# Performance work log

Hardware: AMD Instinct MI355X
Metric: run time of the kernel (lower is better)

The kernel has to match this reference:

```python
import jax, jax.numpy as jnp
import numpy as np

N_NODES = 65536
N_EDGES = 262144
N_GRAPHS = 2048
NF = 16   # num_node_features
EF = 6    # num_edge_features
H1, H2, H3 = 32, 16, 8  # conv1 out, conv2 out, lin1 out


def _lin_init(key, fan_in, fan_out):
    kw, kb = jax.random.split(key)
    s = 1.0 / np.sqrt(fan_in)
    w = jax.random.uniform(kw, (fan_in, fan_out), minval=-s, maxval=s, dtype=jnp.float32)
    b = jax.random.uniform(kb, (fan_out,), minval=-s, maxval=s, dtype=jnp.float32)
    return w, b


def setup_inputs() -> dict:
    key = jax.random.key(0)
    ks = jax.random.split(key, 16)
    inp = {}
    inp["x_p"] = jax.random.normal(ks[0], (N_NODES, NF), dtype=jnp.float32)
    inp["x_d"] = jax.random.normal(ks[1], (4, NF), dtype=jnp.float32)  # unused by forward
    inp["edge_attr_p"] = jax.random.uniform(ks[2], (N_EDGES, EF), dtype=jnp.float32)
    inp["edge_attr_d"] = jax.random.uniform(ks[3], (4, EF), dtype=jnp.float32)  # unused
    inp["edge_index_p"] = jax.random.randint(ks[4], (2, N_EDGES), 0, N_NODES, dtype=jnp.int32)
    inp["x_p_batch"] = jnp.sort(jax.random.randint(ks[5], (N_NODES,), 0, N_GRAPHS, dtype=jnp.int32))
    # conv1: NNConv(NF, 32); edge nn: Linear(EF,16) -> ReLU -> Linear(16, NF*32)
    inp["nn1_w1"], inp["nn1_b1"] = _lin_init(ks[6], EF, 16)
    inp["nn1_w2"], inp["nn1_b2"] = _lin_init(ks[7], 16, NF * H1)
    inp["root1"] = _lin_init(ks[8], NF, H1)[0]
    inp["bias1"] = jnp.zeros((H1,), dtype=jnp.float32)
    # conv2: NNConv(32, 16); edge nn: Linear(EF,16) -> ReLU -> Linear(16, 32*16)
    inp["nn2_w1"], inp["nn2_b1"] = _lin_init(ks[9], EF, 16)
    inp["nn2_w2"], inp["nn2_b2"] = _lin_init(ks[10], 16, H1 * H2)
    inp["root2"] = _lin_init(ks[11], H1, H2)[0]
    inp["bias2"] = jnp.zeros((H2,), dtype=jnp.float32)
    # attention pooling gate: Linear(NF,NF) -> ReLU -> Linear(NF,1)
    inp["gate_w1"], inp["gate_b1"] = _lin_init(ks[12], NF, NF)
    inp["gate_w2"], inp["gate_b2"] = _lin_init(ks[13], NF, 1)
    # head: Linear(16+16, 8) -> Linear(8, 1)  (attention=True)
    inp["lin1_w"], inp["lin1_b"] = _lin_init(ks[14], H2 + NF, H3)
    inp["lin2_w"], inp["lin2_b"] = _lin_init(ks[15], H3, 1)
    return inp


def _nnconv(x, edge_attr, src, dst, w1, b1, w2, b2, root, bias, in_c, out_c, n_nodes):
    # per-edge dynamic weight matrix Theta(e) : [E, in_c, out_c]
    h = jax.nn.relu(edge_attr @ w1 + b1) @ w2 + b2
    w_dyn = h.reshape(-1, in_c, out_c)
    msg = jnp.einsum('ei,eio->eo', x[src], w_dyn)          # [E, out_c]
    agg = jax.ops.segment_sum(msg, dst, num_segments=n_nodes)  # scatter-add
    return agg + x @ root + bias


def _attention_pool(x, batch, gw1, gb1, gw2, gb2, n_graphs):
    g = (jax.nn.relu(x @ gw1 + gb1) @ gw2 + gb2)[:, 0]     # [N] gate logits
    m = jax.ops.segment_max(g, batch, num_segments=n_graphs)
    e = jnp.exp(g - m[batch])
    s = jax.ops.segment_sum(e, batch, num_segments=n_graphs)
    alpha = e / s[batch]                                    # per-graph softmax
    return jax.ops.segment_sum(alpha[:, None] * x, batch, num_segments=n_graphs)


def _mean_pool(x, batch, n_graphs):
    s = jax.ops.segment_sum(x, batch, num_segments=n_graphs)
    cnt = jax.ops.segment_sum(jnp.ones((x.shape[0],), x.dtype), batch, num_segments=n_graphs)
    return s / jnp.maximum(cnt, 1.0)[:, None]


def reference(x_p, x_d, edge_attr_p, edge_attr_d, edge_index_p, x_p_batch,
              nn1_w1, nn1_b1, nn1_w2, nn1_b2, root1, bias1,
              nn2_w1, nn2_b1, nn2_w2, nn2_b2, root2, bias2,
              gate_w1, gate_b1, gate_w2, gate_b2,
              lin1_w, lin1_b, lin2_w, lin2_b):
    src, dst = edge_index_p[0], edge_index_p[1]
    # attention pooling on raw node features (attention=True)
    x_att = _attention_pool(x_p, x_p_batch, gate_w1, gate_b1, gate_w2, gate_b2, N_GRAPHS)
    # two NNConv layers with ReLU
    h = jax.nn.relu(_nnconv(x_p, edge_attr_p, src, dst, nn1_w1, nn1_b1, nn1_w2, nn1_b2,
                            root1, bias1, NF, H1, N_NODES))
    h = jax.nn.relu(_nnconv(h, edge_attr_p, src, dst, nn2_w1, nn2_b1, nn2_w2, nn2_b2,
                            root2, bias2, H1, H2, N_NODES))
    g = _mean_pool(h, x_p_batch, N_GRAPHS)                  # [B, 16]
    g = jnp.concatenate([g, x_att], axis=1)                 # [B, 32]
    # dropout p=0.5 is identity in eval mode
    g = g @ lin1_w + lin1_b
    out = g @ lin2_w + lin2_b                               # [B, 1]
    return out
```

## Files before the change

### kernel.cpp

```cpp
#include <hip/hip_runtime.h>

#define NN 65536
#define NE 262144
#define NG 2048

typedef __attribute__((ext_vector_type(16))) float f32x16;
typedef __attribute__((ext_vector_type(4)))  float f32x4;
typedef __attribute__((ext_vector_type(8)))  __bf16 bf16x8;

__device__ inline unsigned pack2(float a, float b) {
    return __builtin_amdgcn_perm(__float_as_uint(b), __float_as_uint(a), 0x07060302u);
}
__device__ inline float lof(float p) {
    return p - __uint_as_float(__float_as_uint(p) & 0xffff0000u);
}
__device__ inline bf16x8 asb(uint4 u) { return __builtin_bit_cast(bf16x8, u); }

__global__ __launch_bounds__(256) void k_setup(
    const int* __restrict__ batch,
    const float* __restrict__ w2a, const float* __restrict__ b2a,
    const float* __restrict__ w2b, const float* __restrict__ b2c,
    int* __restrict__ cnt, int* __restrict__ cur, int* __restrict__ goffs,
    unsigned* __restrict__ f1, unsigned* __restrict__ f2)
{
    int t = blockIdx.x * 256 + threadIdx.x;
    if (t < NN) { cnt[t] = 0; cur[t] = 0; }
    if (t <= NG) {
        int lo = 0, hi = NN;
        while (lo < hi) {
            int mid = (lo + hi) >> 1;
            if (batch[mid] < t) lo = mid + 1; else hi = mid;
        }
        goffs[t] = lo;
    }
    if (t < 17408) {
        int c = t / 8704;
        int r = t - c * 8704;
        int d = r & 3;
        int l = (r >> 2) & 63;
        int tt = (r >> 8) & 1;
        int s = r >> 9;
        if (c == 0) {
            int n = l & 31, g = l >> 5;
            int j0 = 2*d;
            int c0 = (g*8 + j0)*32 + n;
            int c1 = c0 + 32;
            float a = (s < 16) ? w2a[s*512 + c0] : b2a[c0];
            float b = (s < 16) ? w2a[s*512 + c1] : b2a[c1];
            f1[r] = tt ? pack2(lof(a), lof(b)) : pack2(a, b);
        } else {
            int n = l & 15, g = l >> 4;
            int j0 = 2*d;
            int c0 = (g*8 + j0)*16 + n;
            int c1 = c0 + 16;
            float a = (s < 16) ? w2b[s*512 + c0] : b2c[c0];
            float b = (s < 16) ? w2b[s*512 + c1] : b2c[c1];
            f2[r] = tt ? pack2(lof(a), lof(b)) : pack2(a, b);
        }
    }
}

__global__ __launch_bounds__(64) void k_gateatt(const float* __restrict__ x,
    const float* __restrict__ gw1, const float* __restrict__ gb1,
    const float* __restrict__ gw2, const float* __restrict__ gb2,
    const int* __restrict__ goffs, float* __restrict__ x_att)
{
    __shared__ float sw[256];
    __shared__ float sb[16];
    __shared__ float sw2[16];
    __shared__ float sb2;
    __shared__ float gb[1024];
    const int g = blockIdx.x;
    const int lane = threadIdx.x;
    for (int i = lane; i < 256; i += 64) sw[i] = gw1[i];
    if (lane < 16) { sb[lane] = gb1[lane]; sw2[lane] = gw2[lane]; }
    if (lane == 0) sb2 = gb2[0];
    const int s = goffs[g], e = goffs[g + 1];
    const int cnt = e - s;
    if (cnt <= 0) {
        if (lane < 16) x_att[g*16 + lane] = 0.f;
        return;
    }
    const int cap = cnt < 1024 ? cnt : 1024;
    __syncthreads();
    for (int ii = lane; ii < cap; ii += 64) {
        const float4* xp = (const float4*)(x + (size_t)(s + ii) * 16);
        float xv[16];
#pragma unroll
        for (int i = 0; i < 4; ++i) {
            float4 tt = xp[i];
            xv[4*i] = tt.x; xv[4*i+1] = tt.y; xv[4*i+2] = tt.z; xv[4*i+3] = tt.w;
        }
        float gv = sb2;
#pragma unroll
        for (int j = 0; j < 16; ++j) {
            float a = sb[j];
#pragma unroll
            for (int i = 0; i < 16; ++i) a += xv[i] * sw[i*16 + j];
            gv += fmaxf(a, 0.f) * sw2[j];
        }
        gb[ii] = gv;
    }
    __syncthreads();
    float m = -1e30f;
    for (int ii = lane; ii < cap; ii += 64) m = fmaxf(m, gb[ii]);
#pragma unroll
    for (int d = 32; d; d >>= 1) m = fmaxf(m, __shfl_xor(m, d));
    float sum = 0.f;
    for (int ii = lane; ii < cap; ii += 64) {
        float ev = expf(gb[ii] - m);
        gb[ii] = ev;
        sum += ev;
    }
#pragma unroll
    for (int d = 32; d; d >>= 1) sum += __shfl_xor(sum, d);
    const float inv = 1.f / sum;
    __syncthreads();
    const int f = lane & 15, sub = lane >> 4;
    float acc = 0.f;
    for (int ii = sub; ii < cap; ii += 4)
        acc += gb[ii] * inv * x[(size_t)(s + ii)*16 + f];
    acc += __shfl_xor(acc, 16);
    acc += __shfl_xor(acc, 32);
    if (lane < 16) x_att[g*16 + f] = acc;
}

__global__ __launch_bounds__(256) void k_hist(const int* __restrict__ ei, int* __restrict__ cnt)
{
    int e = blockIdx.x * 256 + threadIdx.x;
    if (e >= NE) return;
    atomicAdd(&cnt[ei[NE + e]], 1);
}

__global__ __launch_bounds__(256) void k_scan_blk(const int* __restrict__ cnt,
    int* __restrict__ offs, int* __restrict__ bsum)
{
    __shared__ int s[256];
    int t = threadIdx.x, b = blockIdx.x;
    int v = cnt[b*256 + t];
    s[t] = v;
    __syncthreads();
#pragma unroll
    for (int d = 1; d < 256; d <<= 1) {
        int add = (t >= d) ? s[t - d] : 0;
        __syncthreads();
        s[t] += add;
        __syncthreads();
    }
    offs[b*256 + t] = s[t] - v;
    if (t == 255) bsum[b] = s[255];
}

__global__ __launch_bounds__(256) void k_scan_top(const int* __restrict__ bsum,
    int* __restrict__ boff)
{
    __shared__ int s[256];
    int t = threadIdx.x;
    int v = bsum[t];
    s[t] = v;
    __syncthreads();
#pragma unroll
    for (int d = 1; d < 256; d <<= 1) {
        int add = (t >= d) ? s[t - d] : 0;
        __syncthreads();
        s[t] += add;
        __syncthreads();
    }
    boff[t] = s[t] - v;
}

__global__ __launch_bounds__(256) void k_scan_add(int* __restrict__ offs,
    const int* __restrict__ boff)
{
    int i = blockIdx.x * 256 + threadIdx.x;
    if (i == 0) offs[NN] = NE;
    if (i >= NN) return;
    offs[i] += boff[i >> 8];
}

__global__ __launch_bounds__(256) void k_scatter(const int* __restrict__ ei,
    const int* __restrict__ offs, int* __restrict__ cur, int2* __restrict__ epair)
{
    int e = blockIdx.x * 256 + threadIdx.x;
    if (e >= NE) return;
    int d = ei[NE + e];
    int pos = offs[d] + atomicAdd(&cur[d], 1);
    epair[pos] = make_int2(e, ei[e]);
}

__global__ __launch_bounds__(256) void k_conv1(
    const float* __restrict__ x, const float* __restrict__ ea,
    const int2* __restrict__ epair,
    const float* __restrict__ w1, const float* __restrict__ b1,
    const unsigned* __restrict__ bfrag, float* __restrict__ msg)
{
    __shared__ uint4 s_tab[17*2*64];
    const int tid  = threadIdx.x;
    for (int i = tid; i < 17*2*64; i += 256) s_tab[i] = ((const uint4*)bfrag)[i];
    __syncthreads();
    const int lane = tid & 63;
    const int wid  = tid >> 6;
    const int m    = lane & 31;
    const int g    = lane >> 5;

    const int tile = blockIdx.x*4 + wid;
    const int p    = tile*32 + m;
    const int2 ep  = epair[p];
    const int e    = ep.x, src = ep.y;

    float xs[8];
    {
        const float4* xp = (const float4*)(x + (size_t)src*16 + g*8);
        float4 aa = xp[0], bb = xp[1];
        xs[0]=aa.x; xs[1]=aa.y; xs[2]=aa.z; xs[3]=aa.w;
        xs[4]=bb.x; xs[5]=bb.y; xs[6]=bb.z; xs[7]=bb.w;
    }
    float h[17];
    {
        const float2 e01 = *(const float2*)(ea + (size_t)e*6);
        const float2 e23 = *(const float2*)(ea + (size_t)e*6 + 2);
        const float2 e45 = *(const float2*)(ea + (size_t)e*6 + 4);
        const float a0=e01.x, a1=e01.y, a2=e23.x, a3=e23.y, a4=e45.x, a5=e45.y;
#pragma unroll
        for (int j = 0; j < 16; ++j) {
            float c = b1[j];
            c += a0*w1[0*16+j]; c += a1*w1[1*16+j]; c += a2*w1[2*16+j];
            c += a3*w1[3*16+j]; c += a4*w1[4*16+j]; c += a5*w1[5*16+j];
            h[j] = fmaxf(c, 0.f);
        }
        h[16] = 1.f;
    }

    f32x16 acc0 = {}, acc1 = {};
#pragma unroll
    for (int s = 0; s < 17; ++s) {
        const float hs = h[s];
        float p0 = hs*xs[0], p1 = hs*xs[1], p2 = hs*xs[2], p3 = hs*xs[3];
        float p4 = hs*xs[4], p5 = hs*xs[5], p6 = hs*xs[6], p7 = hs*xs[7];
        uint4 uh = { pack2(p0,p1), pack2(p2,p3), pack2(p4,p5), pack2(p6,p7) };
        uint4 ul = { pack2(lof(p0),lof(p1)), pack2(lof(p2),lof(p3)),
                     pack2(lof(p4),lof(p5)), pack2(lof(p6),lof(p7)) };
        uint4 wh = s_tab[(s*2+0)*64 + lane];
        uint4 wl = s_tab[(s*2+1)*64 + lane];
        if (s & 1) {
            acc1 = __builtin_amdgcn_mfma_f32_32x32x16_bf16(asb(uh), asb(wh), acc1, 0, 0, 0);
            acc1 = __builtin_amdgcn_mfma_f32_32x32x16_bf16(asb(uh), asb(wl), acc1, 0, 0, 0);
            acc1 = __builtin_amdgcn_mfma_f32_32x32x16_bf16(asb(ul), asb(wh), acc1, 0, 0, 0);
        } else {
            acc0 = __builtin_amdgcn_mfma_f32_32x32x16_bf16(asb(uh), asb(wh), acc0, 0, 0, 0);
            acc0 = __builtin_amdgcn_mfma_f32_32x32x16_bf16(asb(uh), asb(wl), acc0, 0, 0, 0);
            acc0 = __builtin_amdgcn_mfma_f32_32x32x16_bf16(asb(ul), asb(wh), acc0, 0, 0, 0);
        }
    }

    float* mbase = msg + (size_t)tile*32*32;
    const int rb = g*4;
#pragma unroll
    for (int r = 0; r < 16; ++r) {
        int mr = (r&3) + 8*(r>>2) + rb;
        mbase[(size_t)mr*32 + m] = acc0[r] + acc1[r];
    }
}

__global__ __launch_bounds__(256) void k_conv2(
    const float* __restrict__ x, const float* __restrict__ ea,
    const int2* __restrict__ epair,
    const float* __restrict__ w1, const float* __restrict__ b1,
    const unsigned* __restrict__ bfrag, float* __restrict__ msg)
{
    __shared__ uint4 s_tab[17*2*64];
    __shared__ float lt[4][16*21];
    const int tid  = threadIdx.x;
    for (int i = tid; i < 17*2*64; i += 256) s_tab[i] = ((const uint4*)bfrag)[i];
    __syncthreads();
    const int lane = tid & 63;
    const int wid  = tid >> 6;
    const int m    = lane & 15;
    const int g    = lane >> 4;

    const int tile = blockIdx.x*4 + wid;
    const int p    = tile*16 + m;
    const int2 ep  = epair[p];
    const int e    = ep.x, src = ep.y;

    uint4 xh, xl;
    {
        const float4* xp = (const float4*)(x + (size_t)src*32 + g*8);
        float4 aa = xp[0], bb = xp[1];
        xh = (uint4){ pack2(aa.x,aa.y), pack2(aa.z,aa.w), pack2(bb.x,bb.y), pack2(bb.z,bb.w) };
        xl = (uint4){ pack2(lof(aa.x),lof(aa.y)), pack2(lof(aa.z),lof(aa.w)),
                      pack2(lof(bb.x),lof(bb.y)), pack2(lof(bb.z),lof(bb.w)) };
    }
    float h[17];
    {
        const float2 e01 = *(const float2*)(ea + (size_t)e*6);
        const float2 e23 = *(const float2*)(ea + (size_t)e*6 + 2);
        const float2 e45 = *(const float2*)(ea + (size_t)e*6 + 4);
        const float a0=e01.x, a1=e01.y, a2=e23.x, a3=e23.y, a4=e45.x, a5=e45.y;
#pragma unroll
        for (int j = 0; j < 16; ++j) {
            float c = b1[j];
            c += a0*w1[0*16+j]; c += a1*w1[1*16+j]; c += a2*w1[2*16+j];
            c += a3*w1[3*16+j]; c += a4*w1[4*16+j]; c += a5*w1[5*16+j];
            h[j] = fmaxf(c, 0.f);
        }
        h[16] = 1.f;
    }

    f32x4 macc = {};
#pragma unroll
    for (int s = 0; s < 17; ++s) {
        uint4 wh = s_tab[(s*2+0)*64 + lane];
        uint4 wl = s_tab[(s*2+1)*64 + lane];
        f32x4 t = {};
        t = __builtin_amdgcn_mfma_f32_16x16x32_bf16(asb(wh), asb(xh), t, 0, 0, 0);
        t = __builtin_amdgcn_mfma_f32_16x16x32_bf16(asb(wl), asb(xh), t, 0, 0, 0);
        t = __builtin_amdgcn_mfma_f32_16x16x32_bf16(asb(wh), asb(xl), t, 0, 0, 0);
        const float hs = h[s];
        macc.x += hs*t.x; macc.y += hs*t.y; macc.z += hs*t.z; macc.w += hs*t.w;
    }

    float* lw = lt[wid];
    lw[m*21 + g*4 + 0] = macc.x;
    lw[m*21 + g*4 + 1] = macc.y;
    lw[m*21 + g*4 + 2] = macc.z;
    lw[m*21 + g*4 + 3] = macc.w;
    asm volatile("s_waitcnt lgkmcnt(0)" ::: "memory");
    const int rrow = lane >> 2, fq = lane & 3;
    float o0 = lw[rrow*21 + fq*4 + 0];
    float o1 = lw[rrow*21 + fq*4 + 1];
    float o2 = lw[rrow*21 + fq*4 + 2];
    float o3 = lw[rrow*21 + fq*4 + 3];
    float4* mb = (float4*)(msg + (size_t)tile*256);
    mb[rrow*4 + fq] = make_float4(o0, o1, o2, o3);
}

__global__ __launch_bounds__(256) void k_reduce1(
    const float* __restrict__ msg, const int* __restrict__ offs,
    const float* __restrict__ x, const float* __restrict__ root,
    const float* __restrict__ bias, float* __restrict__ h1)
{
    __shared__ float s_r[512];
    __shared__ float s_b[32];
    int tid = threadIdx.x;
    for (int i = tid; i < 512; i += 256) s_r[i] = root[i];
    if (tid < 32) s_b[tid] = bias[tid];
    __syncthreads();
    int gid = blockIdx.x * 256 + tid;
    int n = gid >> 3, q = gid & 7;
    int s = offs[n], e = offs[n + 1];
    float4 acc = make_float4(s_b[4*q], s_b[4*q+1], s_b[4*q+2], s_b[4*q+3]);
    const float4* s_r4 = (const float4*)s_r;
    const float* xp = x + (size_t)n * 16;
#pragma unroll
    for (int i = 0; i < 16; ++i) {
        float xi = xp[i];
        float4 w = s_r4[i*8 + q];
        acc.x += xi*w.x; acc.y += xi*w.y; acc.z += xi*w.z; acc.w += xi*w.w;
    }
    for (int p = s; p < e; ++p) {
        float4 mr = ((const float4*)(msg + (size_t)p * 32))[q];
        acc.x += mr.x; acc.y += mr.y; acc.z += mr.z; acc.w += mr.w;
    }
    acc.x = fmaxf(acc.x, 0.f); acc.y = fmaxf(acc.y, 0.f);
    acc.z = fmaxf(acc.z, 0.f); acc.w = fmaxf(acc.w, 0.f);
    ((float4*)(h1 + (size_t)n * 32))[q] = acc;
}

__global__ __launch_bounds__(256) void k_reduce2(
    const float* __restrict__ msg, const int* __restrict__ offs,
    const float* __restrict__ h1, const float* __restrict__ root,
    const float* __restrict__ bias, float* __restrict__ h2)
{
    __shared__ float s_r[512];
    __shared__ float s_b[16];
    int tid = threadIdx.x;
    for (int i = tid; i < 512; i += 256) s_r[i] = root[i];
    if (tid < 16) s_b[tid] = bias[tid];
    __syncthreads();
    int gid = blockIdx.x * 256 + tid;
    int n = gid >> 2, q = gid & 3;
    int s = offs[n], e = offs[n + 1];
    float4 acc = make_float4(s_b[4*q], s_b[4*q+1], s_b[4*q+2], s_b[4*q+3]);
    const float4* s_r4 = (const float4*)s_r;
    const float* xp = h1 + (size_t)n * 32;
#pragma unroll
    for (int i = 0; i < 32; ++i) {
        float xi = xp[i];
        float4 w = s_r4[i*4 + q];
        acc.x += xi*w.x; acc.y += xi*w.y; acc.z += xi*w.z; acc.w += xi*w.w;
    }
    for (int p = s; p < e; ++p) {
        float4 mr = ((const float4*)(msg + (size_t)p * 16))[q];
        acc.x += mr.x; acc.y += mr.y; acc.z += mr.z; acc.w += mr.w;
    }
    acc.x = fmaxf(acc.x, 0.f); acc.y = fmaxf(acc.y, 0.f);
    acc.z = fmaxf(acc.z, 0.f); acc.w = fmaxf(acc.w, 0.f);
    ((float4*)(h2 + (size_t)n * 16))[q] = acc;
}

__global__ __launch_bounds__(64) void k_head(
    const float* __restrict__ h2, const float* __restrict__ x_att,
    const int* __restrict__ goffs,
    const float* __restrict__ l1w, const float* __restrict__ l1b,
    const float* __restrict__ l2w, const float* __restrict__ l2b,
    float* __restrict__ out)
{
    int g = blockIdx.x;
    int lane = threadIdx.x;
    int s = goffs[g], e = goffs[g + 1];
    __shared__ float v[32];
    __shared__ float hmid[8];
    int f = lane & 15, sub = lane >> 4;
    float acc = 0.f;
    for (int i = s + sub; i < e; i += 4) acc += h2[(size_t)i*16 + f];
    acc += __shfl_xor(acc, 16);
    acc += __shfl_xor(acc, 32);
    float cnt = fmaxf((float)(e - s), 1.0f);
    if (lane < 16) {
        v[lane]      = acc / cnt;
        v[16 + lane] = x_att[g*16 + lane];
    }
    __syncthreads();
    if (lane < 8) {
        float a = l1b[lane];
#pragma unroll
        for (int i = 0; i < 32; ++i) a += v[i] * l1w[i*8 + lane];
        hmid[lane] = a;
    }
    __syncthreads();
    if (lane == 0) {
        float a = l2b[0];
#pragma unroll
        for (int j = 0; j < 8; ++j) a += hmid[j] * l2w[j];
        out[g] = a;
    }
}

extern "C" void kernel_launch(void* const* d_in, const int* in_sizes, int n_in,
                              void* d_out, int out_size, void* d_ws, size_t ws_size,
                              hipStream_t stream) {
    const float* x_p    = (const float*)d_in[0];
    const float* ea_p   = (const float*)d_in[2];
    const int*   ei     = (const int*)d_in[4];
    const int*   batch  = (const int*)d_in[5];
    const float* nn1_w1 = (const float*)d_in[6];
    const float* nn1_b1 = (const float*)d_in[7];
    const float* nn1_w2 = (const float*)d_in[8];
    const float* nn1_b2 = (const float*)d_in[9];
    const float* root1  = (const float*)d_in[10];
    const float* bias1  = (const float*)d_in[11];
    const float* nn2_w1 = (const float*)d_in[12];
    const float* nn2_b1 = (const float*)d_in[13];
    const float* nn2_w2 = (const float*)d_in[14];
    const float* nn2_b2 = (const float*)d_in[15];
    const float* root2  = (const float*)d_in[16];
    const float* bias2  = (const float*)d_in[17];
    const float* gw1    = (const float*)d_in[18];
    const float* gb1    = (const float*)d_in[19];
    const float* gw2    = (const float*)d_in[20];
    const float* gb2    = (const float*)d_in[21];
    const float* l1w    = (const float*)d_in[22];
    const float* l1b    = (const float*)d_in[23];
    const float* l2w    = (const float*)d_in[24];
    const float* l2b    = (const float*)d_in[25];

    float*    h1     = (float*)d_ws;
    float*    h2     = h1 + (size_t)NN * 32;
    float*    x_att  = h2 + (size_t)NN * 16;
    int*      goffs  = (int*)(x_att + (size_t)NG * 16);
    int*      offs   = goffs + 2052;
    int*      cnt    = offs + 65540;
    int*      cur    = cnt + NN;
    int*      bsum   = cur + NN;
    int*      boff   = bsum + 256;
    int2*     epair  = (int2*)(boff + 256);
    unsigned* bfrag1 = (unsigned*)(epair + NE);
    unsigned* bfrag2 = bfrag1 + 8704;
    float*    msg    = (float*)(bfrag2 + 8704);

    k_setup<<<512, 256, 0, stream>>>(batch, nn1_w2, nn1_b2, nn2_w2, nn2_b2,
                                     cnt, cur, goffs, bfrag1, bfrag2);

    k_gateatt<<<NG, 64, 0, stream>>>(x_p, gw1, gb1, gw2, gb2, goffs, x_att);

    k_hist<<<NE/256, 256, 0, stream>>>(ei, cnt);
    k_scan_blk<<<NN/256, 256, 0, stream>>>(cnt, offs, bsum);
    k_scan_top<<<1, 256, 0, stream>>>(bsum, boff);
    k_scan_add<<<NN/256, 256, 0, stream>>>(offs, boff);
    k_scatter<<<NE/256, 256, 0, stream>>>(ei, offs, cur, epair);

    k_conv1<<<2048, 256, 0, stream>>>(x_p, ea_p, epair, nn1_w1, nn1_b1, bfrag1, msg);
    k_reduce1<<<NN*8/256, 256, 0, stream>>>(msg, offs, x_p, root1, bias1, h1);

    k_conv2<<<4096, 256, 0, stream>>>(h1, ea_p, epair, nn2_w1, nn2_b1, bfrag2, msg);
    k_reduce2<<<NN*4/256, 256, 0, stream>>>(msg, offs, h1, root2, bias2, h2);

    k_head<<<NG, 64, 0, stream>>>(h2, x_att, goffs, l1w, l1b, l2w, l2b, (float*)d_out);
}
```

Baseline: 136.4 us.

## Fuse edge message and per-node reduction in shared memory, merge histogram and scan

Each conv kernel now keeps its per-edge messages in shared memory and reduces them per destination node within the block. Nodes whose edges lie entirely inside the block's edge range are finished in place (root term, bias, ReLU). Boundary nodes are accumulated with atomics into a zeroed buffer and finished by a separate fix-up kernel. This removes the global msg buffer write and readback; the histogram is folded into the gate-attention kernel and the three-pass scan becomes a single-block scan, cutting launches. The costs are binary searches per block, float atomics for split nodes, zeroing two accumulation buffers, and a serial single-block scan.

Measured after the change: 189.4 us. 1.39x slower.

```diff
diff --git a/kernel.cpp b/kernel.cpp
--- a/kernel.cpp
+++ b/kernel.cpp
@@ -21,10 +21,18 @@
     const float* __restrict__ w2a, const float* __restrict__ b2a,
     const float* __restrict__ w2b, const float* __restrict__ b2c,
     int* __restrict__ cnt, int* __restrict__ cur, int* __restrict__ goffs,
+    float* __restrict__ agg1, float* __restrict__ agg2,
     unsigned* __restrict__ f1, unsigned* __restrict__ f2)
 {
     int t = blockIdx.x * 256 + threadIdx.x;
     if (t < NN) { cnt[t] = 0; cur[t] = 0; }
+    {
+        float4 z = make_float4(0.f, 0.f, 0.f, 0.f);
+        float4* a1 = (float4*)agg1;
+        float4* a2 = (float4*)agg2;
+        for (int i = t; i < NN*8; i += 131072) a1[i] = z;
+        for (int i = t; i < NN*4; i += 131072) a2[i] = z;
+    }
     if (t <= NG) {
         int lo = 0, hi = NN;
         while (lo < hi) {
@@ -61,10 +69,16 @@
 }
 
 __global__ __launch_bounds__(64) void k_gateatt(const float* __restrict__ x,
+    const int* __restrict__ ei, int* __restrict__ cnt,
     const float* __restrict__ gw1, const float* __restrict__ gb1,
     const float* __restrict__ gw2, const float* __restrict__ gb2,
     const int* __restrict__ goffs, float* __restrict__ x_att)
 {
+    {
+        int gid = blockIdx.x * 64 + threadIdx.x;
+        for (int e = gid; e < NE; e += NG*64)
+            atomicAdd(&cnt[ei[NE + e]], 1);
+    }
     __shared__ float sw[256];
     __shared__ float sb[16];
     __shared__ float sw2[16];
@@ -76,12 +90,12 @@
     if (lane < 16) { sb[lane] = gb1[lane]; sw2[lane] = gw2[lane]; }
     if (lane == 0) sb2 = gb2[0];
     const int s = goffs[g], e = goffs[g + 1];
-    const int cnt = e - s;
-    if (cnt <= 0) {
+    const int cntg = e - s;
+    if (cntg <= 0) {
         if (lane < 16) x_att[g*16 + lane] = 0.f;
         return;
     }
-    const int cap = cnt < 1024 ? cnt : 1024;
+    const int cap = cntg < 1024 ? cntg : 1024;
     __syncthreads();
     for (int ii = lane; ii < cap; ii += 64) {
         const float4* xp = (const float4*)(x + (size_t)(s + ii) * 16);
@@ -125,57 +139,31 @@
     if (lane < 16) x_att[g*16 + f] = acc;
 }
 
-__global__ __launch_bounds__(256) void k_hist(const int* __restrict__ ei, int* __restrict__ cnt)
-{
-    int e = blockIdx.x * 256 + threadIdx.x;
-    if (e >= NE) return;
-    atomicAdd(&cnt[ei[NE + e]], 1);
-}
-
-__global__ __launch_bounds__(256) void k_scan_blk(const int* __restrict__ cnt,
-    int* __restrict__ offs, int* __restrict__ bsum)
-{
-    __shared__ int s[256];
-    int t = threadIdx.x, b = blockIdx.x;
-    int v = cnt[b*256 + t];
-    s[t] = v;
-    __syncthreads();
-#pragma unroll
-    for (int d = 1; d < 256; d <<= 1) {
-        int add = (t >= d) ? s[t - d] : 0;
+__global__ __launch_bounds__(1024) void k_scan(const int* __restrict__ cnt,
+    int* __restrict__ offs)
+{
+    __shared__ int ls[1024];
+    const int t = threadIdx.x;
+    const int base = t * 64;
+    int sum = 0;
+#pragma unroll 8
+    for (int i = 0; i < 64; ++i) sum += cnt[base + i];
+    ls[t] = sum;
+    __syncthreads();
+    for (int d = 1; d < 1024; d <<= 1) {
+        int add = (t >= d) ? ls[t - d] : 0;
         __syncthreads();
-        s[t] += add;
+        ls[t] += add;
         __syncthreads();
     }
-    offs[b*256 + t] = s[t] - v;
-    if (t == 255) bsum[b] = s[255];
-}
-
-__global__ __launch_bounds__(256) void k_scan_top(const int* __restrict__ bsum,
-    int* __restrict__ boff)
-{
-    __shared__ int s[256];
-    int t = threadIdx.x;
-    int v = bsum[t];
-    s[t] = v;
-    __syncthreads();
-#pragma unroll
-    for (int d = 1; d < 256; d <<= 1) {
-        int add = (t >= d) ? s[t - d] : 0;
-        __syncthreads();
-        s[t] += add;
-        __syncthreads();
-    }
-    boff[t] = s[t] - v;
-}
-
-__global__ __launch_bounds__(256) void k_scan_add(int* __restrict__ offs,
-    const int* __restrict__ boff)
-{
-    int i = blockIdx.x * 256 + threadIdx.x;
-    if (i == 0) offs[NN] = NE;
-    if (i >= NN) return;
-    offs[i] += boff[i >> 8];
+    int run = ls[t] - sum;
+#pragma unroll 8
+    for (int i = 0; i < 64; ++i) {
+        int c = cnt[base + i];
+        offs[base + i] = run;
+        run += c;
+    }
+    if (t == 1023) offs[NN] = run;
 }
 
 __global__ __launch_bounds__(256) void k_scatter(const int* __restrict__ ei,
@@ -188,155 +176,148 @@
     epair[pos] = make_int2(e, ei[e]);
 }
 
-__global__ __launch_bounds__(256) void k_conv1(
+__global__ __launch_bounds__(256) void k_layer1(
     const float* __restrict__ x, const float* __restrict__ ea,
-    const int2* __restrict__ epair,
+    const int2* __restrict__ epair, const int* __restrict__ offs,
     const float* __restrict__ w1, const float* __restrict__ b1,
-    const unsigned* __restrict__ bfrag, float* __restrict__ msg)
+    const unsigned* __restrict__ bfrag,
+    const float* __restrict__ root, const float* __restrict__ bias,
+    float* __restrict__ h1, float* __restrict__ agg1)
 {
     __shared__ uint4 s_tab[17*2*64];
+    __shared__ float s_msg[128*32];
+    __shared__ float s_r[512];
+    __shared__ float s_bias[32];
+    __shared__ int   s_nlo, s_nhi;
     const int tid  = threadIdx.x;
     for (int i = tid; i < 17*2*64; i += 256) s_tab[i] = ((const uint4*)bfrag)[i];
-    __syncthreads();
-    const int lane = tid & 63;
-    const int wid  = tid >> 6;
-    const int m    = lane & 31;
-    const int g    = lane >> 5;
-
-    const int tile = blockIdx.x*4 + wid;
-    const int p    = tile*32 + m;
-    const int2 ep  = epair[p];
-    const int e    = ep.x, src = ep.y;
-
-    float xs[8];
+    for (int i = tid; i < 512; i += 256) s_r[i] = root[i];
+    if (tid < 32) s_bias[tid] = bias[tid];
+    const int P0 = blockIdx.x * 128;
+    if (tid == 0) {
+        int lo = 0, hi = NN;
+        while (lo < hi) { int mid = (lo+hi)>>1; if (offs[mid+1] <= P0) lo = mid+1; else hi = mid; }
+        s_nlo = lo;
+        lo = 0; hi = NN;
+        int PL = P0 + 127;
+        while (lo < hi) { int mid = (lo+hi)>>1; if (offs[mid+1] <= PL) lo = mid+1; else hi = mid; }
+        s_nhi = lo;
+    }
+    __syncthreads();
+
     {
-        const float4* xp = (const float4*)(x + (size_t)src*16 + g*8);
-        float4 aa = xp[0], bb = xp[1];
-        xs[0]=aa.x; xs[1]=aa.y; xs[2]=aa.z; xs[3]=aa.w;
-        xs[4]=bb.x; xs[5]=bb.y; xs[6]=bb.z; xs[7]=bb.w;
-    }
-    float h[17];
+        const int lane = tid & 63;
+        const int wid  = tid >> 6;
+        const int m    = lane & 31;
+        const int g    = lane >> 5;
+        const int p    = P0 + wid*32 + m;
+        const int2 ep  = epair[p];
+        const int e    = ep.x, src = ep.y;
+
+        float xs[8];
+        {
+            const float4* xp = (const float4*)(x + (size_t)src*16 + g*8);
+            float4 aa = xp[0], bb = xp[1];
+            xs[0]=aa.x; xs[1]=aa.y; xs[2]=aa.z; xs[3]=aa.w;
+            xs[4]=bb.x; xs[5]=bb.y; xs[6]=bb.z; xs[7]=bb.w;
+        }
+        float h[17];
+        {
+            const float2 e01 = *(const float2*)(ea + (size_t)e*6);
+            const float2 e23 = *(const float2*)(ea + (size_t)e*6 + 2);
+            const float2 e45 = *(const float2*)(ea + (size_t)e*6 + 4);
+            const float a0=e01.x, a1=e01.y, a2=e23.x, a3=e23.y, a4=e45.x, a5=e45.y;
+#pragma unroll
+            for (int j = 0; j < 16; ++j) {
+                float c = b1[j];
+                c += a0*w1[0*16+j]; c += a1*w1[1*16+j]; c += a2*w1[2*16+j];
+                c += a3*w1[3*16+j]; c += a4*w1[4*16+j]; c += a5*w1[5*16+j];
+                h[j] = fmaxf(c, 0.f);
+            }
+            h[16] = 1.f;
+        }
+
+        f32x16 acc0 = {}, acc1 = {};
+#pragma unroll
+        for (int s = 0; s < 17; ++s) {
+            const float hs = h[s];
+            float p0 = hs*xs[0], p1 = hs*xs[1], p2 = hs*xs[2], p3 = hs*xs[3];
+            float p4 = hs*xs[4], p5 = hs*xs[5], p6 = hs*xs[6], p7 = hs*xs[7];
+            uint4 uh = { pack2(p0,p1), pack2(p2,p3), pack2(p4,p5), pack2(p6,p7) };
+            uint4 ul = { pack2(lof(p0),lof(p1)), pack2(lof(p2),lof(p3)),
+                         pack2(lof(p4),lof(p5)), pack2(lof(p6),lof(p7)) };
+            uint4 wh = s_tab[(s*2+0)*64 + lane];
+            uint4 wl = s_tab[(s*2+1)*64 + lane];
+            if (s & 1) {
+                acc1 = __builtin_amdgcn_mfma_f32_32x32x16_bf16(asb(uh), asb(wh), acc1, 0, 0, 0);
+                acc1 = __builtin_amdgcn_mfma_f32_32x32x16_bf16(asb(uh), asb(wl), acc1, 0, 0, 0);
+                acc1 = __builtin_amdgcn_mfma_f32_32x32x16_bf16(asb(ul), asb(wh), acc1, 0, 0, 0);
+            } else {
+                acc0 = __builtin_amdgcn_mfma_f32_32x32x16_bf16(asb(uh), asb(wh), acc0, 0, 0, 0);
+                acc0 = __builtin_amdgcn_mfma_f32_32x32x16_bf16(asb(uh), asb(wl), acc0, 0, 0, 0);
+                acc0 = __builtin_amdgcn_mfma_f32_32x32x16_bf16(asb(ul), asb(wh), acc0, 0, 0, 0);
+            }
+        }
+        float* mbase = s_msg + wid*32*32;
+        const int rb = g*4;
+#pragma unroll
+        for (int r = 0; r < 16; ++r) {
+            int mr = (r&3) + 8*(r>>2) + rb;
+            mbase[mr*32 + m] = acc0[r] + acc1[r];
+        }
+    }
+    __syncthreads();
+
     {
-        const float2 e01 = *(const float2*)(ea + (size_t)e*6);
-        const float2 e23 = *(const float2*)(ea + (size_t)e*6 + 2);
-        const float2 e45 = *(const float2*)(ea + (size_t)e*6 + 4);
-        const float a0=e01.x, a1=e01.y, a2=e23.x, a3=e23.y, a4=e45.x, a5=e45.y;
-#pragma unroll
-        for (int j = 0; j < 16; ++j) {
-            float c = b1[j];
-            c += a0*w1[0*16+j]; c += a1*w1[1*16+j]; c += a2*w1[2*16+j];
-            c += a3*w1[3*16+j]; c += a4*w1[4*16+j]; c += a5*w1[5*16+j];
-            h[j] = fmaxf(c, 0.f);
-        }
-        h[16] = 1.f;
-    }
-
-    f32x16 acc0 = {}, acc1 = {};
-#pragma unroll
-    for (int s = 0; s < 17; ++s) {
-        const float hs = h[s];
-        float p0 = hs*xs[0], p1 = hs*xs[1], p2 = hs*xs[2], p3 = hs*xs[3];
-        float p4 = hs*xs[4], p5 = hs*xs[5], p6 = hs*xs[6], p7 = hs*xs[7];
-        uint4 uh = { pack2(p0,p1), pack2(p2,p3), pack2(p4,p5), pack2(p6,p7) };
-        uint4 ul = { pack2(lof(p0),lof(p1)), pack2(lof(p2),lof(p3)),
-                     pack2(lof(p4),lof(p5)), pack2(lof(p6),lof(p7)) };
-        uint4 wh = s_tab[(s*2+0)*64 + lane];
-        uint4 wl = s_tab[(s*2+1)*64 + lane];
-        if (s & 1) {
-            acc1 = __builtin_amdgcn_mfma_f32_32x32x16_bf16(asb(uh), asb(wh), acc1, 0, 0, 0);
-            acc1 = __builtin_amdgcn_mfma_f32_32x32x16_bf16(asb(uh), asb(wl), acc1, 0, 0, 0);
-            acc1 = __builtin_amdgcn_mfma_f32_32x32x16_bf16(asb(ul), asb(wh), acc1, 0, 0, 0);
-        } else {
-            acc0 = __builtin_amdgcn_mfma_f32_32x32x16_bf16(asb(uh), asb(wh), acc0, 0, 0, 0);
-            acc0 = __builtin_amdgcn_mfma_f32_32x32x16_bf16(asb(uh), asb(wl), acc0, 0, 0, 0);
-            acc0 = __builtin_amdgcn_mfma_f32_32x32x16_bf16(asb(ul), asb(wh), acc0, 0, 0, 0);
-        }
-    }
-
-    float* mbase = msg + (size_t)tile*32*32;
-    const int rb = g*4;
-#pragma unroll
-    for (int r = 0; r < 16; ++r) {
-        int mr = (r&3) + 8*(r>>2) + rb;
-        mbase[(size_t)mr*32 + m] = acc0[r] + acc1[r];
-    }
-}
-
-__global__ __launch_bounds__(256) void k_conv2(
-    const float* __restrict__ x, const float* __restrict__ ea,
-    const int2* __restrict__ epair,
-    const float* __restrict__ w1, const float* __restrict__ b1,
-    const unsigned* __restrict__ bfrag, float* __restrict__ msg)
-{
-    __shared__ uint4 s_tab[17*2*64];
-    __shared__ float lt[4][16*21];
-    const int tid  = threadIdx.x;
-    for (int i = tid; i < 17*2*64; i += 256) s_tab[i] = ((const uint4*)bfrag)[i];
-    __syncthreads();
-    const int lane = tid & 63;
-    const int wid  = tid >> 6;
-    const int m    = lane & 15;
-    const int g    = lane >> 4;
-
-    const int tile = blockIdx.x*4 + wid;
-    const int p    = tile*16 + m;
-    const int2 ep  = epair[p];
-    const int e    = ep.x, src = ep.y;
-
-    uint4 xh, xl;
-    {
-        const float4* xp = (const float4*)(x + (size_t)src*32 + g*8);
-        float4 aa = xp[0], bb = xp[1];
-        xh = (uint4){ pack2(aa.x,aa.y), pack2(aa.z,aa.w), pack2(bb.x,bb.y), pack2(bb.z,bb.w) };
-        xl = (uint4){ pack2(lof(aa.x),lof(aa.y)), pack2(lof(aa.z),lof(aa.w)),
-                      pack2(lof(bb.x),lof(bb.y)), pack2(lof(bb.z),lof(bb.w)) };
-    }
-    float h[17];
-    {
-        const float2 e01 = *(const float2*)(ea + (size_t)e*6);
-        const float2 e23 = *(const float2*)(ea + (size_t)e*6 + 2);
-        const float2 e45 = *(const float2*)(ea + (size_t)e*6 + 4);
-        const float a0=e01.x, a1=e01.y, a2=e23.x, a3=e23.y, a4=e45.x, a5=e45.y;
-#pragma unroll
-        for (int j = 0; j < 16; ++j) {
-            float c = b1[j];
-            c += a0*w1[0*16+j]; c += a1*w1[1*16+j]; c += a2*w1[2*16+j];
-            c += a3*w1[3*16+j]; c += a4*w1[4*16+j]; c += a5*w1[5*16+j];
-            h[j] = fmaxf(c, 0.f);
-        }
-        h[16] = 1.f;
-    }
-
-    f32x4 macc = {};
-#pragma unroll
-    for (int s = 0; s < 17; ++s) {
-        uint4 wh = s_tab[(s*2+0)*64 + lane];
-        uint4 wl = s_tab[(s*2+1)*64 + lane];
-        f32x4 t = {};
-        t = __builtin_amdgcn_mfma_f32_16x16x32_bf16(asb(wh), asb(xh), t, 0, 0, 0);
-        t = __builtin_amdgcn_mfma_f32_16x16x32_bf16(asb(wl), asb(xh), t, 0, 0, 0);
-        t = __builtin_amdgcn_mfma_f32_16x16x32_bf16(asb(wh), asb(xl), t, 0, 0, 0);
-        const float hs = h[s];
-        macc.x += hs*t.x; macc.y += hs*t.y; macc.z += hs*t.z; macc.w += hs*t.w;
-    }
-
-    float* lw = lt[wid];
-    lw[m*21 + g*4 + 0] = macc.x;
-    lw[m*21 + g*4 + 1] = macc.y;
-    lw[m*21 + g*4 + 2] = macc.z;
-    lw[m*21 + g*4 + 3] = macc.w;
-    asm volatile("s_waitcnt lgkmcnt(0)" ::: "memory");
-    const int rrow = lane >> 2, fq = lane & 3;
-    float o0 = lw[rrow*21 + fq*4 + 0];
-    float o1 = lw[rrow*21 + fq*4 + 1];
-    float o2 = lw[rrow*21 + fq*4 + 2];
-    float o3 = lw[rrow*21 + fq*4 + 3];
-    float4* mb = (float4*)(msg + (size_t)tile*256);
-    mb[rrow*4 + fq] = make_float4(o0, o1, o2, o3);
-}
-
-__global__ __launch_bounds__(256) void k_reduce1(
-    const float* __restrict__ msg, const int* __restrict__ offs,
+        const int nlo = s_nlo, nhi = s_nhi;
+        const int items = (nhi - nlo + 1) * 8;
+        const float4* s_r4 = (const float4*)s_r;
+        const float4* m4 = (const float4*)s_msg;
+        for (int it = tid; it < items; it += 256) {
+            const int n = nlo + (it >> 3);
+            const int q = it & 7;
+            const int os = offs[n], oe = offs[n+1];
+            const int ss = os > P0 ? os : P0;
+            const int se = oe < P0+128 ? oe : P0+128;
+            if (ss >= se) continue;
+            float4 acc = make_float4(0.f, 0.f, 0.f, 0.f);
+            for (int p = ss; p < se; ++p) {
+                float4 mr = m4[(p - P0)*8 + q];
+                acc.x += mr.x; acc.y += mr.y; acc.z += mr.z; acc.w += mr.w;
+            }
+            const bool interior = (os >= P0) && (oe <= P0 + 128);
+            if (interior) {
+                acc.x += s_bias[4*q]; acc.y += s_bias[4*q+1];
+                acc.z += s_bias[4*q+2]; acc.w += s_bias[4*q+3];
+                const float4* xp4 = (const float4*)(x + (size_t)n * 16);
+#pragma unroll
+                for (int ii = 0; ii < 4; ++ii) {
+                    float4 xv = xp4[ii];
+                    float4 w0 = s_r4[(ii*4+0)*8 + q];
+                    float4 w1v = s_r4[(ii*4+1)*8 + q];
+                    float4 w2v = s_r4[(ii*4+2)*8 + q];
+                    float4 w3 = s_r4[(ii*4+3)*8 + q];
+                    acc.x += xv.x*w0.x + xv.y*w1v.x + xv.z*w2v.x + xv.w*w3.x;
+                    acc.y += xv.x*w0.y + xv.y*w1v.y + xv.z*w2v.y + xv.w*w3.y;
+                    acc.z += xv.x*w0.z + xv.y*w1v.z + xv.z*w2v.z + xv.w*w3.z;
+                    acc.w += xv.x*w0.w + xv.y*w1v.w + xv.z*w2v.w + xv.w*w3.w;
+                }
+                acc.x = fmaxf(acc.x, 0.f); acc.y = fmaxf(acc.y, 0.f);
+                acc.z = fmaxf(acc.z, 0.f); acc.w = fmaxf(acc.w, 0.f);
+                ((float4*)(h1 + (size_t)n * 32))[q] = acc;
+            } else {
+                float* ap = agg1 + (size_t)n * 32 + q*4;
+                atomicAdd(ap + 0, acc.x);
+                atomicAdd(ap + 1, acc.y);
+                atomicAdd(ap + 2, acc.z);
+                atomicAdd(ap + 3, acc.w);
+            }
+        }
+    }
+}
+
+__global__ __launch_bounds__(256) void k_fix1(
+    const int* __restrict__ offs, const float* __restrict__ agg1,
     const float* __restrict__ x, const float* __restrict__ root,
     const float* __restrict__ bias, float* __restrict__ h1)
 {
@@ -348,27 +329,162 @@
     __syncthreads();
     int gid = blockIdx.x * 256 + tid;
     int n = gid >> 3, q = gid & 7;
-    int s = offs[n], e = offs[n + 1];
-    float4 acc = make_float4(s_b[4*q], s_b[4*q+1], s_b[4*q+2], s_b[4*q+3]);
+    int os = offs[n], oe = offs[n+1];
+    bool interior = (oe > os) && ((os >> 7) == ((oe - 1) >> 7));
+    if (interior) return;
+    float4 acc = ((const float4*)(agg1 + (size_t)n * 32))[q];
+    acc.x += s_b[4*q]; acc.y += s_b[4*q+1]; acc.z += s_b[4*q+2]; acc.w += s_b[4*q+3];
     const float4* s_r4 = (const float4*)s_r;
-    const float* xp = x + (size_t)n * 16;
-#pragma unroll
-    for (int i = 0; i < 16; ++i) {
-        float xi = xp[i];
-        float4 w = s_r4[i*8 + q];
-        acc.x += xi*w.x; acc.y += xi*w.y; acc.z += xi*w.z; acc.w += xi*w.w;
-    }
-    for (int p = s; p < e; ++p) {
-        float4 mr = ((const float4*)(msg + (size_t)p * 32))[q];
-        acc.x += mr.x; acc.y += mr.y; acc.z += mr.z; acc.w += mr.w;
+    const float4* xp4 = (const float4*)(x + (size_t)n * 16);
+#pragma unroll
+    for (int ii = 0; ii < 4; ++ii) {
+        float4 xv = xp4[ii];
+        float4 w0 = s_r4[(ii*4+0)*8 + q];
+        float4 w1v = s_r4[(ii*4+1)*8 + q];
+        float4 w2v = s_r4[(ii*4+2)*8 + q];
+        float4 w3 = s_r4[(ii*4+3)*8 + q];
+        acc.x += xv.x*w0.x + xv.y*w1v.x + xv.z*w2v.x + xv.w*w3.x;
+        acc.y += xv.x*w0.y + xv.y*w1v.y + xv.z*w2v.y + xv.w*w3.y;
+        acc.z += xv.x*w0.z + xv.y*w1v.z + xv.z*w2v.z + xv.w*w3.z;
+        acc.w += xv.x*w0.w + xv.y*w1v.w + xv.z*w2v.w + xv.w*w3.w;
     }
     acc.x = fmaxf(acc.x, 0.f); acc.y = fmaxf(acc.y, 0.f);
     acc.z = fmaxf(acc.z, 0.f); acc.w = fmaxf(acc.w, 0.f);
     ((float4*)(h1 + (size_t)n * 32))[q] = acc;
 }
 
-__global__ __launch_bounds__(256) void k_reduce2(
-    const float* __restrict__ msg, const int* __restrict__ offs,
+__global__ __launch_bounds__(256) void k_layer2(
+    const float* __restrict__ x, const float* __restrict__ ea,
+    const int2* __restrict__ epair, const int* __restrict__ offs,
+    const float* __restrict__ w1, const float* __restrict__ b1,
+    const unsigned* __restrict__ bfrag,
+    const float* __restrict__ root, const float* __restrict__ bias,
+    float* __restrict__ h2, float* __restrict__ agg2)
+{
+    __shared__ uint4 s_tab[17*2*64];
+    __shared__ float s_msg[64*16];
+    __shared__ float s_r[512];
+    __shared__ float s_bias[16];
+    __shared__ int   s_nlo, s_nhi;
+    const int tid  = threadIdx.x;
+    for (int i = tid; i < 17*2*64; i += 256) s_tab[i] = ((const uint4*)bfrag)[i];
+    for (int i = tid; i < 512; i += 256) s_r[i] = root[i];
+    if (tid < 16) s_bias[tid] = bias[tid];
+    const int P0 = blockIdx.x * 64;
+    if (tid == 0) {
+        int lo = 0, hi = NN;
+        while (lo < hi) { int mid = (lo+hi)>>1; if (offs[mid+1] <= P0) lo = mid+1; else hi = mid; }
+        s_nlo = lo;
+        lo = 0; hi = NN;
+        int PL = P0 + 63;
+        while (lo < hi) { int mid = (lo+hi)>>1; if (offs[mid+1] <= PL) lo = mid+1; else hi = mid; }
+        s_nhi = lo;
+    }
+    __syncthreads();
+
+    {
+        const int lane = tid & 63;
+        const int wid  = tid >> 6;
+        const int m    = lane & 15;
+        const int g    = lane >> 4;
+        const int p    = P0 + wid*16 + m;
+        const int2 ep  = epair[p];
+        const int e    = ep.x, src = ep.y;
+
+        uint4 xh, xl;
+        {
+            const float4* xp = (const float4*)(x + (size_t)src*32 + g*8);
+            float4 aa = xp[0], bb = xp[1];
+            xh = (uint4){ pack2(aa.x,aa.y), pack2(aa.z,aa.w), pack2(bb.x,bb.y), pack2(bb.z,bb.w) };
+            xl = (uint4){ pack2(lof(aa.x),lof(aa.y)), pack2(lof(aa.z),lof(aa.w)),
+                          pack2(lof(bb.x),lof(bb.y)), pack2(lof(bb.z),lof(bb.w)) };
+        }
+        float h[17];
+        {
+            const float2 e01 = *(const float2*)(ea + (size_t)e*6);
+            const float2 e23 = *(const float2*)(ea + (size_t)e*6 + 2);
+            const float2 e45 = *(const float2*)(ea + (size_t)e*6 + 4);
+            const float a0=e01.x, a1=e01.y, a2=e23.x, a3=e23.y, a4=e45.x, a5=e45.y;
+#pragma unroll
+            for (int j = 0; j < 16; ++j) {
+                float c = b1[j];
+                c += a0*w1[0*16+j]; c += a1*w1[1*16+j]; c += a2*w1[2*16+j];
+                c += a3*w1[3*16+j]; c += a4*w1[4*16+j]; c += a5*w1[5*16+j];
+                h[j] = fmaxf(c, 0.f);
+            }
+            h[16] = 1.f;
+        }
+
+        f32x4 macc = {};
+#pragma unroll
+        for (int s = 0; s < 17; ++s) {
+            uint4 wh = s_tab[(s*2+0)*64 + lane];
+            uint4 wl = s_tab[(s*2+1)*64 + lane];
+            f32x4 t = {};
+            t = __builtin_amdgcn_mfma_f32_16x16x32_bf16(asb(wh), asb(xh), t, 0, 0, 0);
+            t = __builtin_amdgcn_mfma_f32_16x16x32_bf16(asb(wl), asb(xh), t, 0, 0, 0);
+            t = __builtin_amdgcn_mfma_f32_16x16x32_bf16(asb(wh), asb(xl), t, 0, 0, 0);
+            const float hs = h[s];
+            macc.x += hs*t.x; macc.y += hs*t.y; macc.z += hs*t.z; macc.w += hs*t.w;
+        }
+        float* lw = s_msg + (wid*16 + m)*16;
+        lw[g*4 + 0] = macc.x;
+        lw[g*4 + 1] = macc.y;
+        lw[g*4 + 2] = macc.z;
+        lw[g*4 + 3] = macc.w;
+    }
+    __syncthreads();
+
+    {
+        const int nlo = s_nlo, nhi = s_nhi;
+        const int items = (nhi - nlo + 1) * 4;
+        const float4* s_r4 = (const float4*)s_r;
+        const float4* m4 = (const float4*)s_msg;
+        for (int it = tid; it < items; it += 256) {
+            const int n = nlo + (it >> 2);
+            const int q = it & 3;
+            const int os = offs[n], oe = offs[n+1];
+            const int ss = os > P0 ? os : P0;
+            const int se = oe < P0+64 ? oe : P0+64;
+            if (ss >= se) continue;
+            float4 acc = make_float4(0.f, 0.f, 0.f, 0.f);
+            for (int p = ss; p < se; ++p) {
+                float4 mr = m4[(p - P0)*4 + q];
+                acc.x += mr.x; acc.y += mr.y; acc.z += mr.z; acc.w += mr.w;
+            }
+            const bool interior = (os >= P0) && (oe <= P0 + 64);
+            if (interior) {
+                acc.x += s_bias[4*q]; acc.y += s_bias[4*q+1];
+                acc.z += s_bias[4*q+2]; acc.w += s_bias[4*q+3];
+                const float4* xp4 = (const float4*)(x + (size_t)n * 32);
+#pragma unroll
+                for (int ii = 0; ii < 8; ++ii) {
+                    float4 xv = xp4[ii];
+                    float4 w0 = s_r4[(ii*4+0)*4 + q];
+                    float4 w1v = s_r4[(ii*4+1)*4 + q];
+                    float4 w2v = s_r4[(ii*4+2)*4 + q];
+                    float4 w3 = s_r4[(ii*4+3)*4 + q];
+                    acc.x += xv.x*w0.x + xv.y*w1v.x + xv.z*w2v.x + xv.w*w3.x;
+                    acc.y += xv.x*w0.y + xv.y*w1v.y + xv.z*w2v.y + xv.w*w3.y;
+                    acc.z += xv.x*w0.z + xv.y*w1v.z + xv.z*w2v.z + xv.w*w3.z;
+                    acc.w += xv.x*w0.w + xv.y*w1v.w + xv.z*w2v.w + xv.w*w3.w;
+                }
+                acc.x = fmaxf(acc.x, 0.f); acc.y = fmaxf(acc.y, 0.f);
+                acc.z = fmaxf(acc.z, 0.f); acc.w = fmaxf(acc.w, 0.f);
+                ((float4*)(h2 + (size_t)n * 16))[q] = acc;
+            } else {
+                float* ap = agg2 + (size_t)n * 16 + q*4;
+                atomicAdd(ap + 0, acc.x);
+                atomicAdd(ap + 1, acc.y);
+                atomicAdd(ap + 2, acc.z);
+                atomicAdd(ap + 3, acc.w);
+            }
+        }
+    }
+}
+
+__global__ __launch_bounds__(256) void k_fix2(
+    const int* __restrict__ offs, const float* __restrict__ agg2,
     const float* __restrict__ h1, const float* __restrict__ root,
     const float* __restrict__ bias, float* __restrict__ h2)
 {
@@ -380,19 +496,24 @@
     __syncthreads();
     int gid = blockIdx.x * 256 + tid;
     int n = gid >> 2, q = gid & 3;
-    int s = offs[n], e = offs[n + 1];
-    float4 acc = make_float4(s_b[4*q], s_b[4*q+1], s_b[4*q+2], s_b[4*q+3]);
+    int os = offs[n], oe = offs[n+1];
+    bool interior = (oe > os) && ((os >> 6) == ((oe - 1) >> 6));
+    if (interior) return;
+    float4 acc = ((const float4*)(agg2 + (size_t)n * 16))[q];
+    acc.x += s_b[4*q]; acc.y += s_b[4*q+1]; acc.z += s_b[4*q+2]; acc.w += s_b[4*q+3];
     const float4* s_r4 = (const float4*)s_r;
-    const float* xp = h1 + (size_t)n * 32;
-#pragma unroll
-    for (int i = 0; i < 32; ++i) {
-        float xi = xp[i];
-        float4 w = s_r4[i*4 + q];
-        acc.x += xi*w.x; acc.y += xi*w.y; acc.z += xi*w.z; acc.w += xi*w.w;
-    }
-    for (int p = s; p < e; ++p) {
-        float4 mr = ((const float4*)(msg + (size_t)p * 16))[q];
-        acc.x += mr.x; acc.y += mr.y; acc.z += mr.z; acc.w += mr.w;
+    const float4* xp4 = (const float4*)(h1 + (size_t)n * 32);
+#pragma unroll
+    for (int ii = 0; ii < 8; ++ii) {
+        float4 xv = xp4[ii];
+        float4 w0 = s_r4[(ii*4+0)*4 + q];
+        float4 w1v = s_r4[(ii*4+1)*4 + q];
+        float4 w2v = s_r4[(ii*4+2)*4 + q];
+        float4 w3 = s_r4[(ii*4+3)*4 + q];
+        acc.x += xv.x*w0.x + xv.y*w1v.x + xv.z*w2v.x + xv.w*w3.x;
+        acc.y += xv.x*w0.y + xv.y*w1v.y + xv.z*w2v.y + xv.w*w3.y;
+        acc.z += xv.x*w0.z + xv.y*w1v.z + xv.z*w2v.z + xv.w*w3.z;
+        acc.w += xv.x*w0.w + xv.y*w1v.w + xv.z*w2v.w + xv.w*w3.w;
     }
     acc.x = fmaxf(acc.x, 0.f); acc.y = fmaxf(acc.y, 0.f);
     acc.z = fmaxf(acc.z, 0.f); acc.w = fmaxf(acc.w, 0.f);
@@ -467,34 +588,27 @@
 
     float*    h1     = (float*)d_ws;
     float*    h2     = h1 + (size_t)NN * 32;
-    float*    x_att  = h2 + (size_t)NN * 16;
+    float*    agg1   = h2 + (size_t)NN * 16;
+    float*    agg2   = agg1 + (size_t)NN * 32;
+    float*    x_att  = agg2 + (size_t)NN * 16;
     int*      goffs  = (int*)(x_att + (size_t)NG * 16);
     int*      offs   = goffs + 2052;
     int*      cnt    = offs + 65540;
     int*      cur    = cnt + NN;
-    int*      bsum   = cur + NN;
-    int*      boff   = bsum + 256;
-    int2*     epair  = (int2*)(boff + 256);
+    int2*     epair  = (int2*)(cur + NN);
     unsigned* bfrag1 = (unsigned*)(epair + NE);
     unsigned* bfrag2 = bfrag1 + 8704;
-    float*    msg    = (float*)(bfrag2 + 8704);
 
     k_setup<<<512, 256, 0, stream>>>(batch, nn1_w2, nn1_b2, nn2_w2, nn2_b2,
-                                     cnt, cur, goffs, bfrag1, bfrag2);
-
-    k_gateatt<<<NG, 64, 0, stream>>>(x_p, gw1, gb1, gw2, gb2, goffs, x_att);
-
-    k_hist<<<NE/256, 256, 0, stream>>>(ei, cnt);
-    k_scan_blk<<<NN/256, 256, 0, stream>>>(cnt, offs, bsum);
-    k_scan_top<<<1, 256, 0, stream>>>(bsum, boff);
-    k_scan_add<<<NN/256, 256, 0, stream>>>(offs, boff);
+                                     cnt, cur, goffs, agg1, agg2, bfrag1, bfrag2);
+    k_gateatt<<<NG, 64, 0, stream>>>(x_p, ei, cnt, gw1, gb1, gw2, gb2, goffs, x_att);
+    k_scan<<<1, 1024, 0, stream>>>(cnt, offs);
     k_scatter<<<NE/256, 256, 0, stream>>>(ei, offs, cur, epair);
-
-    k_conv1<<<2048, 256, 0, stream>>>(x_p, ea_p, epair, nn1_w1, nn1_b1, bfrag1, msg);
-    k_reduce1<<<NN*8/256, 256, 0, stream>>>(msg, offs, x_p, root1, bias1, h1);
-
-    k_conv2<<<4096, 256, 0, stream>>>(h1, ea_p, epair, nn2_w1, nn2_b1, bfrag2, msg);
-    k_reduce2<<<NN*4/256, 256, 0, stream>>>(msg, offs, h1, root2, bias2, h2);
-
+    k_layer1<<<NE/128, 256, 0, stream>>>(x_p, ea_p, epair, offs,
+                                         nn1_w1, nn1_b1, bfrag1, root1, bias1, h1, agg1);
+    k_fix1<<<NN*8/256, 256, 0, stream>>>(offs, agg1, x_p, root1, bias1, h1);
+    k_layer2<<<NE/64, 256, 0, stream>>>(h1, ea_p, epair, offs,
+                                        nn2_w1, nn2_b1, bfrag2, root2, bias2, h2, agg2);
+    k_fix2<<<NN*4/256, 256, 0, stream>>>(offs, agg2, h1, root2, bias2, h2);
     k_head<<<NG, 64, 0, stream>>>(h2, x_att, goffs, l1w, l1b, l2w, l2b, (float*)d_out);
 }
```
